# Optimization experiments

Measured on AMD Instinct MI355X. Metric: run time of the kernel, lower is better.

## Reference

```python
import jax, jax.numpy as jnp
import numpy as np

N, E = 40000, 640000
EMB, HID, H, TXT = 128, 128, 4, 384
C = HID // H  # per-head channels = 32


def _prelu(x, a):
    return jnp.where(x >= 0, x, a * x)


def _layernorm(x, g, b, eps=1e-5):
    m = jnp.mean(x, axis=-1, keepdims=True)
    v = jnp.mean((x - m) ** 2, axis=-1, keepdims=True)
    return (x - m) / jnp.sqrt(v + eps) * g + b


def _gat_conv(h, src, dst, W, att_src, att_dst, bias):
    # PyG GATConv (concat=True, eval mode): lin has no bias, self-loops already in src/dst.
    xh = (h @ W.T).reshape(N, H, C)                      # [N,H,C]
    a_src = jnp.sum(xh * att_src, axis=-1)               # [N,H]
    a_dst = jnp.sum(xh * att_dst, axis=-1)               # [N,H]
    alpha = jax.nn.leaky_relu(a_src[src] + a_dst[dst], negative_slope=0.2)  # [Et,H]
    amax = jax.ops.segment_max(alpha, dst, num_segments=N)
    ex = jnp.exp(alpha - amax[dst])
    denom = jax.ops.segment_sum(ex, dst, num_segments=N)
    coef = ex / denom[dst]                               # scatter-softmax over dst
    out = jax.ops.segment_sum(xh[src] * coef[:, :, None], dst, num_segments=N)
    return out.reshape(N, H * C) + bias


def setup_inputs() -> dict:
    key = jax.random.key(0)
    ks = jax.random.split(key, 20)
    nrm = lambda k, s, sc=0.05: jax.random.normal(k, s, jnp.float32) * sc
    inp = {
        "x": nrm(ks[0], (N, EMB), 1.0),
        "num_x": nrm(ks[1], (N, 1), 1.0),
        "num_mask": jnp.ones((N,), jnp.float32),
        "txt_x": nrm(ks[2], (N, TXT), 1.0),
        "txt_mask": jnp.ones((N,), jnp.float32),
        "edge_index": jax.random.randint(ks[3], (2, E), 0, N, jnp.int32),
        "num_proj_w": nrm(ks[4], (EMB, 1)), "num_proj_b": jnp.zeros((EMB,), jnp.float32),
        "txt_proj_w": nrm(ks[5], (EMB, TXT)), "txt_proj_b": jnp.zeros((EMB,), jnp.float32),
        "node_proj_w": nrm(ks[6], (HID, EMB)), "node_proj_b": jnp.zeros((HID,), jnp.float32),
        "prelu0_a": jnp.full((HID,), 0.25, jnp.float32),
        "conv1_w": nrm(ks[7], (HID, HID)), "att_src1": nrm(ks[8], (H, C)), "att_dst1": nrm(ks[9], (H, C)), "bias1": jnp.zeros((HID,), jnp.float32),
        "norm1_g": jnp.ones((HID,), jnp.float32), "norm1_b": jnp.zeros((HID,), jnp.float32),
        "prelu1_a": jnp.full((HID,), 0.25, jnp.float32),
        "conv2_w": nrm(ks[10], (HID, HID)), "att_src2": nrm(ks[11], (H, C)), "att_dst2": nrm(ks[12], (H, C)), "bias2": jnp.zeros((HID,), jnp.float32),
        "norm2_g": jnp.ones((HID,), jnp.float32), "norm2_b": jnp.zeros((HID,), jnp.float32),
        "prelu2_a": jnp.full((HID,), 0.25, jnp.float32),
        "out_w": nrm(ks[13], (1, HID)), "out_b": jnp.zeros((1,), jnp.float32),
    }
    return inp


def reference(x, num_x, num_mask, txt_x, txt_mask, edge_index,
              num_proj_w, num_proj_b, txt_proj_w, txt_proj_b,
              node_proj_w, node_proj_b, prelu0_a,
              conv1_w, att_src1, att_dst1, bias1, norm1_g, norm1_b, prelu1_a,
              conv2_w, att_src2, att_dst2, bias2, norm2_g, norm2_b, prelu2_a,
              out_w, out_b):
    # add self loops (PyG GATConv default)
    loop = jnp.arange(N, dtype=edge_index.dtype)
    src = jnp.concatenate([edge_index[0], loop])
    dst = jnp.concatenate([edge_index[1], loop])

    h = (num_x * num_mask[:, None]) @ num_proj_w.T + num_proj_b
    h = h + (txt_x * txt_mask[:, None]) @ txt_proj_w.T + txt_proj_b
    h = h + x @ node_proj_w.T + node_proj_b
    h = _prelu(h, prelu0_a)

    h = _gat_conv(h, src, dst, conv1_w, att_src1, att_dst1, bias1)
    h = _prelu(_layernorm(h, norm1_g, norm1_b), prelu1_a)  # dropout: eval mode -> identity

    h = _gat_conv(h, src, dst, conv2_w, att_src2, att_dst2, bias2)
    h = _prelu(_layernorm(h, norm2_g, norm2_b), prelu2_a)

    return (h @ out_w.T + out_b).squeeze(-1)  # [N]
```

## Files before the change

### kernel.cpp

```cpp
#include <hip/hip_runtime.h>
#include <stdint.h>

typedef unsigned short u16;
typedef unsigned int u32;
typedef __attribute__((ext_vector_type(8))) short bf16x8;
typedef __attribute__((ext_vector_type(4))) float f32x4;

__device__ __forceinline__ float bf2f(u32 u) {
    union { u32 i; float f; } v; v.i = u << 16; return v.f;
}
__device__ __forceinline__ u16 f2bf(float f) {
    u32 x = __float_as_uint(f);
    return (u16)((x + 0x7fffu + ((x >> 16) & 1u)) >> 16);
}
__device__ __forceinline__ float wred_sum(float v) {
#pragma unroll
    for (int o = 32; o > 0; o >>= 1) v += __shfl_xor(v, o, 64);
    return v;
}
__device__ __forceinline__ bf16x8 cvt8(float4 a, float4 b) {
    union { uint4 u; bf16x8 v; } t;
    t.u.x = (u32)f2bf(a.x) | ((u32)f2bf(a.y) << 16);
    t.u.y = (u32)f2bf(a.z) | ((u32)f2bf(a.w) << 16);
    t.u.z = (u32)f2bf(b.x) | ((u32)f2bf(b.y) << 16);
    t.u.w = (u32)f2bf(b.z) | ((u32)f2bf(b.w) << 16);
    return t.v;
}
__device__ __forceinline__ bf16x8 ld16B(const u16* p, size_t off) {
    union { uint4 u; bf16x8 b; } t; t.u = *(const uint4*)(p + off); return t.b;
}
__device__ __forceinline__ bf16x8 ldB(const u16* sw, int ct, int ks, int l16, int quad) {
    union { uint4 u; bf16x8 b; } t;
    t.u = *(const uint4*)&sw[(ct * 16 + l16) * 136 + ks * 32 + quad * 8];
    return t.b;
}
__device__ __forceinline__ void ldW8(const u16* __restrict__ W, int ldk, int koff,
                                     int tid, uint4* r) {
#pragma unroll
    for (int it = 0; it < 8; ++it) {
        int idx = (it * 256 + tid) * 8;
        int row = idx >> 7, kk = idx & 127;
        r[it] = *(const uint4*)(W + (size_t)row * ldk + koff + kk);
    }
}
__device__ __forceinline__ void stW8(u16* sw, int tid, const uint4* r) {
#pragma unroll
    for (int it = 0; it < 8; ++it) {
        int idx = (it * 256 + tid) * 8;
        int row = idx >> 7, kk = idx & 127;
        *(uint4*)&sw[row * 136 + kk] = r[it];
    }
}
__device__ __forceinline__ void ldA8(const float* __restrict__ p, float4* r) {
#pragma unroll
    for (int ks = 0; ks < 4; ++ks) {
        r[ks * 2]     = *(const float4*)(p + ks * 32);
        r[ks * 2 + 1] = *(const float4*)(p + ks * 32 + 4);
    }
}

__global__ void k_cvtw(const float* __restrict__ s0, const float* __restrict__ s1,
                       const float* __restrict__ s2, const float* __restrict__ s3,
                       u16* __restrict__ d, int n0, int n1, int n2, int n3) {
    int i = (blockIdx.x * 256 + threadIdx.x) * 8;
    int t = i;
    const float* s;
    if (t < n0) s = s0 + t;
    else if ((t -= n0) < n1) s = s1 + t;
    else if ((t -= n1) < n2) s = s2 + t;
    else if ((t -= n2) < n3) s = s3 + t;
    else return;
    float4 a = *(const float4*)s, b = *(const float4*)(s + 4);
    uint4 v;
    v.x = (u32)f2bf(a.x) | ((u32)f2bf(a.y) << 16);
    v.y = (u32)f2bf(a.z) | ((u32)f2bf(a.w) << 16);
    v.z = (u32)f2bf(b.x) | ((u32)f2bf(b.y) << 16);
    v.w = (u32)f2bf(b.z) | ((u32)f2bf(b.w) << 16);
    *(uint4*)(d + i) = v;
}

__global__ void k_zero(int* __restrict__ p, int n) {
    int i = blockIdx.x * 256 + threadIdx.x;
    if (i < n) p[i] = 0;
}
__global__ void k_hist(const int* __restrict__ dst, int E, int* __restrict__ deg) {
    int e = blockIdx.x * 256 + threadIdx.x;
    if (e < E) atomicAdd(&deg[dst[e]], 1);
}
__global__ __launch_bounds__(1024) void k_scanA(const int* __restrict__ deg, int n,
                                                int* __restrict__ out, int* __restrict__ bsum) {
    __shared__ int wsum[16];
    int t = threadIdx.x, w = t >> 6, lane = t & 63;
    int i0 = blockIdx.x * 4096 + t * 4;
    int4 v = make_int4(0, 0, 0, 0);
    if (i0 + 3 < n) v = *(const int4*)&deg[i0];
    else {
        if (i0 < n)     v.x = deg[i0];
        if (i0 + 1 < n) v.y = deg[i0 + 1];
        if (i0 + 2 < n) v.z = deg[i0 + 2];
    }
    int tsum = v.x + v.y + v.z + v.w;
    int s = tsum;
#pragma unroll
    for (int o = 1; o < 64; o <<= 1) { int u = __shfl_up(s, o, 64); if (lane >= o) s += u; }
    if (lane == 63) wsum[w] = s;
    __syncthreads();
    if (w == 0 && lane < 16) {
        int ws = wsum[lane];
#pragma unroll
        for (int o = 1; o < 16; o <<= 1) { int u = __shfl_up(ws, o, 64); if (lane >= o) ws += u; }
        wsum[lane] = ws;
    }
    __syncthreads();
    int woff = (w == 0) ? 0 : wsum[w - 1];
    int p = woff + s - tsum;
    if (i0 + 3 < n) {
        int4 o4; o4.x = p; o4.y = p + v.x; o4.z = p + v.x + v.y; o4.w = p + v.x + v.y + v.z;
        *(int4*)&out[i0] = o4;
    } else {
        int pp = p;
        if (i0 < n)     { out[i0] = pp;     pp += v.x; }
        if (i0 + 1 < n) { out[i0 + 1] = pp; pp += v.y; }
        if (i0 + 2 < n) { out[i0 + 2] = pp; }
    }
    if (t == 0) bsum[blockIdx.x] = wsum[15];
}
__global__ void k_scanB(int* __restrict__ bsum, int nb, int* __restrict__ total) {
    int lane = threadIdx.x;
    int v = (lane < nb) ? bsum[lane] : 0;
    int s = v;
#pragma unroll
    for (int o = 1; o < 64; o <<= 1) { int u = __shfl_up(s, o, 64); if (lane >= o) s += u; }
    if (lane < nb) bsum[lane] = s - v;
    if (lane == 63) total[0] = s;
}
__global__ void k_scanC(int* __restrict__ rowptr, int* __restrict__ cursor,
                        const int* __restrict__ boff, int n) {
    int i = blockIdx.x * 256 + threadIdx.x;
    if (i < n) {
        int r = rowptr[i] + boff[i >> 12];
        rowptr[i] = r; cursor[i] = r;
    }
}
__global__ void k_scatter(const int* __restrict__ srcp, const int* __restrict__ dstp, int E,
                          int* __restrict__ cursor, int* __restrict__ col) {
    int e = blockIdx.x * 256 + threadIdx.x;
    if (e < E) {
        int p = atomicAdd(&cursor[dstp[e]], 1);
        col[p] = srcp[e];
    }
}

__global__ __launch_bounds__(256, 1) void k_fused1(
    const float* __restrict__ x, const float* __restrict__ numx, const float* __restrict__ numm,
    const float* __restrict__ txt, const float* __restrict__ txtm,
    const float* __restrict__ numw, const float* __restrict__ numb,
    const float* __restrict__ txtb, const float* __restrict__ nodeb,
    const float* __restrict__ pa,
    const u16* __restrict__ txtwb, const u16* __restrict__ nodewb, const u16* __restrict__ w1b,
    const float* __restrict__ atts, const float* __restrict__ attd,
    u16* __restrict__ xh, float* __restrict__ asrc, float* __restrict__ adst) {
    __shared__ u16 sw[128 * 136];
    __shared__ u16 sh[4][16 * 136];
    int tid = threadIdx.x, w = tid >> 6, lane = tid & 63, quad = lane >> 4, l16 = lane & 15;
    int nb = blockIdx.x * 64 + w * 16;

    const float* trow = txt + (size_t)(nb + l16) * 384 + quad * 8;
    const float* xrow = x + (size_t)(nb + l16) * 128 + quad * 8;

    f32x4 acc[8];
#pragma unroll
    for (int ct = 0; ct < 8; ++ct) { f32x4 z = {0.f, 0.f, 0.f, 0.f}; acc[ct] = z; }

    auto compute = [&](const float4* A) {
#pragma unroll
        for (int ks = 0; ks < 4; ++ks) {
            bf16x8 a0 = cvt8(A[ks * 2], A[ks * 2 + 1]);
#pragma unroll
            for (int ct = 0; ct < 8; ++ct)
                acc[ct] = __builtin_amdgcn_mfma_f32_16x16x32_bf16(
                    a0, ldB(sw, ct, ks, l16, quad), acc[ct], 0, 0, 0);
        }
    };

    uint4 w0[8], w1[8], w2[8];
    float4 aC[8], aN[8];

    ldW8(txtwb, 384, 0, tid, w0);
    ldW8(txtwb, 384, 128, tid, w1);
    ldA8(trow, aC);

    stW8(sw, tid, w0);
    __syncthreads();
    ldW8(txtwb, 384, 256, tid, w2);
    ldA8(trow + 128, aN);
    compute(aC);
    __syncthreads();

    stW8(sw, tid, w1);
    __syncthreads();
    ldW8(nodewb, 128, 0, tid, w0);
    ldA8(trow + 256, aC);
    compute(aN);
    __syncthreads();

    stW8(sw, tid, w2);
    __syncthreads();
    ldW8(w1b, 128, 0, tid, w1);
    ldA8(xrow, aN);
    compute(aC);
#pragma unroll
    for (int r = 0; r < 4; ++r) {
        float tm = txtm[nb + quad * 4 + r];
#pragma unroll
        for (int ct = 0; ct < 8; ++ct) acc[ct][r] *= tm;
    }
    __syncthreads();

    stW8(sw, tid, w0);
    __syncthreads();
    compute(aN);

    float nm[4];
#pragma unroll
    for (int r = 0; r < 4; ++r) {
        int n = nb + quad * 4 + r;
        nm[r] = numx[n] * numm[n];
    }
#pragma unroll
    for (int ct = 0; ct < 8; ++ct) {
        int c = ct * 16 + l16;
        float cw = numw[c];
        float cb = numb[c] + txtb[c] + nodeb[c];
        float pav = pa[c];
#pragma unroll
        for (int r = 0; r < 4; ++r) {
            float v = acc[ct][r] + nm[r] * cw + cb;
            v = v >= 0.f ? v : pav * v;
            sh[w][(quad * 4 + r) * 136 + c] = f2bf(v);
        }
    }
    __syncthreads();
    stW8(sw, tid, w1);
    __syncthreads();
    f32x4 a2[8];
#pragma unroll
    for (int ct = 0; ct < 8; ++ct) { f32x4 z = {0.f, 0.f, 0.f, 0.f}; a2[ct] = z; }
#pragma unroll
    for (int ks = 0; ks < 4; ++ks) {
        bf16x8 a0 = ld16B(sh[w], l16 * 136 + ks * 32 + quad * 8);
#pragma unroll
        for (int ct = 0; ct < 8; ++ct)
            a2[ct] = __builtin_amdgcn_mfma_f32_16x16x32_bf16(
                a0, ldB(sw, ct, ks, l16, quad), a2[ct], 0, 0, 0);
    }
#pragma unroll
    for (int ct = 0; ct < 8; ++ct) {
        int c = ct * 16 + l16;
#pragma unroll
        for (int r = 0; r < 4; ++r)
            xh[(size_t)(nb + quad * 4 + r) * 128 + c] = f2bf(a2[ct][r]);
    }
    float as_[8], ad_[8];
#pragma unroll
    for (int ct = 0; ct < 8; ++ct) {
        int c = ct * 16 + l16;
        as_[ct] = atts[c];
        ad_[ct] = attd[c];
    }
#pragma unroll
    for (int hh = 0; hh < 4; ++hh) {
        float vs[4], vd[4];
#pragma unroll
        for (int r = 0; r < 4; ++r) {
            vs[r] = a2[2 * hh][r] * as_[2 * hh] + a2[2 * hh + 1][r] * as_[2 * hh + 1];
            vd[r] = a2[2 * hh][r] * ad_[2 * hh] + a2[2 * hh + 1][r] * ad_[2 * hh + 1];
        }
#pragma unroll
        for (int o = 1; o <= 8; o <<= 1) {
#pragma unroll
            for (int r = 0; r < 4; ++r) {
                vs[r] += __shfl_xor(vs[r], o, 64);
                vd[r] += __shfl_xor(vd[r], o, 64);
            }
        }
        if ((l16 >> 2) == hh) {
            int r = l16 & 3;
            float ss = (r == 0) ? vs[0] : (r == 1) ? vs[1] : (r == 2) ? vs[2] : vs[3];
            float dd = (r == 0) ? vd[0] : (r == 1) ? vd[1] : (r == 2) ? vd[2] : vd[3];
            int n = nb + quad * 4 + r;
            asrc[n * 4 + hh] = ss;
            adst[n * 4 + hh] = dd;
        }
    }
}

__global__ __launch_bounds__(256) void k_xh(
    const u16* __restrict__ h, const u16* __restrict__ Wb,
    const float* __restrict__ att_s, const float* __restrict__ att_d,
    u16* __restrict__ xh, float* __restrict__ asrc, float* __restrict__ adst) {
    __shared__ u16 sw[128 * 136];
    int tid = threadIdx.x;
    int w = tid >> 6, lane = tid & 63, quad = lane >> 4, l16 = lane & 15;
    int nb = blockIdx.x * 64 + w * 16;
    uint4 wr[8];
    ldW8(Wb, 128, 0, tid, wr);
    uint4 Ar[4];
    const u16* hrow = h + (size_t)(nb + l16) * 128;
#pragma unroll
    for (int ks = 0; ks < 4; ++ks) Ar[ks] = *(const uint4*)(hrow + ks * 32 + quad * 8);
    f32x4 acc[8];
#pragma unroll
    for (int ct = 0; ct < 8; ++ct) { f32x4 z = {0.f, 0.f, 0.f, 0.f}; acc[ct] = z; }
    stW8(sw, tid, wr);
    __syncthreads();
#pragma unroll
    for (int ks = 0; ks < 4; ++ks) {
        union { uint4 u; bf16x8 b; } t; t.u = Ar[ks];
#pragma unroll
        for (int ct = 0; ct < 8; ++ct)
            acc[ct] = __builtin_amdgcn_mfma_f32_16x16x32_bf16(
                t.b, ldB(sw, ct, ks, l16, quad), acc[ct], 0, 0, 0);
    }
#pragma unroll
    for (int ct = 0; ct < 8; ++ct) {
        int c = ct * 16 + l16;
#pragma unroll
        for (int r = 0; r < 4; ++r) {
            int n = nb + quad * 4 + r;
            xh[(size_t)n * 128 + c] = f2bf(acc[ct][r]);
        }
    }
    float as_[8], ad_[8];
#pragma unroll
    for (int ct = 0; ct < 8; ++ct) {
        int c = ct * 16 + l16;
        as_[ct] = att_s[c];
        ad_[ct] = att_d[c];
    }
#pragma unroll
    for (int hh = 0; hh < 4; ++hh) {
        float vs[4], vd[4];
#pragma unroll
        for (int r = 0; r < 4; ++r) {
            vs[r] = acc[2 * hh][r] * as_[2 * hh] + acc[2 * hh + 1][r] * as_[2 * hh + 1];
            vd[r] = acc[2 * hh][r] * ad_[2 * hh] + acc[2 * hh + 1][r] * ad_[2 * hh + 1];
        }
#pragma unroll
        for (int o = 1; o <= 8; o <<= 1) {
#pragma unroll
            for (int r = 0; r < 4; ++r) {
                vs[r] += __shfl_xor(vs[r], o, 64);
                vd[r] += __shfl_xor(vd[r], o, 64);
            }
        }
        if ((l16 >> 2) == hh) {
            int r = l16 & 3;
            float ss = (r == 0) ? vs[0] : (r == 1) ? vs[1] : (r == 2) ? vs[2] : vs[3];
            float dd = (r == 0) ? vd[0] : (r == 1) ? vd[1] : (r == 2) ? vd[2] : vd[3];
            int n = nb + quad * 4 + r;
            asrc[n * 4 + hh] = ss;
            adst[n * 4 + hh] = dd;
        }
    }
}

__global__ __launch_bounds__(64) void k_agg(
    const u16* __restrict__ xh, const float* __restrict__ asrc, const float* __restrict__ adst,
    const int* __restrict__ rowptr, const int* __restrict__ col,
    const float* __restrict__ bias, const float* __restrict__ g, const float* __restrict__ b,
    const float* __restrict__ pa, u16* __restrict__ hnext,
    const float* __restrict__ outw, const float* __restrict__ outb, float* __restrict__ outy,
    int is_final) {
    __shared__ int   scol[64];
    __shared__ float scoef[64][4];
    int n = blockIdx.x, lane = threadIdx.x;
    int beg = rowptr[n], end = rowptr[n + 1];
    const float4* asrc4 = (const float4*)asrc;

    float4 adv = ((const float4*)adst)[n];
    float ad[4] = { adv.x, adv.y, adv.z, adv.w };
    float4 asv = asrc4[n];
    float els[4];
#pragma unroll
    for (int h = 0; h < 4; h++) {
        float a = ((const float*)&asv)[h] + ad[h];
        a = a >= 0.f ? a : 0.2f * a;
        els[h] = __expf(a);
    }
    int hh = lane >> 4;
    u32 vself = ((const u32*)(xh + (size_t)n * 128))[lane];
    float ac0[8], ac1[8];
#pragma unroll
    for (int q = 0; q < 8; ++q) { ac0[q] = 0.f; ac1[q] = 0.f; }
    ac0[0] = els[hh] * bf2f(vself & 0xffffu);
    ac1[0] = els[hh] * bf2f(vself >> 16);
    float l[4] = { 0.f, 0.f, 0.f, 0.f };

    for (int base = beg; base < end; base += 64) {
        int e = base + lane;
        int cnt = min(64, end - base);
        if (e < end) {
            int s = col[e];
            float4 av = asrc4[s];
            scol[lane] = s;
            float cf[4];
#pragma unroll
            for (int h = 0; h < 4; h++) {
                float a = ((const float*)&av)[h] + ad[h];
                a = a >= 0.f ? a : 0.2f * a;
                cf[h] = __expf(a);
                l[h] += cf[h];
            }
            *(float4*)scoef[lane] = make_float4(cf[0], cf[1], cf[2], cf[3]);
        }
        __syncthreads();
        int j = 0;
        for (; j + 7 < cnt; j += 8) {
            int ss[8]; float cc[8]; u32 vv[8];
#pragma unroll
            for (int q = 0; q < 8; ++q) { ss[q] = scol[j + q]; cc[q] = scoef[j + q][hh]; }
#pragma unroll
            for (int q = 0; q < 8; ++q) vv[q] = ((const u32*)(xh + (size_t)ss[q] * 128))[lane];
#pragma unroll
            for (int q = 0; q < 8; ++q) {
                ac0[q] += cc[q] * bf2f(vv[q] & 0xffffu);
                ac1[q] += cc[q] * bf2f(vv[q] >> 16);
            }
        }
        for (; j + 3 < cnt; j += 4) {
            int ss[4]; float cc[4]; u32 vv[4];
#pragma unroll
            for (int q = 0; q < 4; ++q) { ss[q] = scol[j + q]; cc[q] = scoef[j + q][hh]; }
#pragma unroll
            for (int q = 0; q < 4; ++q) vv[q] = ((const u32*)(xh + (size_t)ss[q] * 128))[lane];
#pragma unroll
            for (int q = 0; q < 4; ++q) {
                ac0[q] += cc[q] * bf2f(vv[q] & 0xffffu);
                ac1[q] += cc[q] * bf2f(vv[q] >> 16);
            }
        }
        for (; j < cnt; ++j) {
            int s0 = scol[j];
            float c0 = scoef[j][hh];
            u32 v0 = ((const u32*)(xh + (size_t)s0 * 128))[lane];
            ac0[0] += c0 * bf2f(v0 & 0xffffu);
            ac1[0] += c0 * bf2f(v0 >> 16);
        }
        __syncthreads();
    }
    float acc0 = 0.f, acc1 = 0.f;
#pragma unroll
    for (int q = 0; q < 8; ++q) { acc0 += ac0[q]; acc1 += ac1[q]; }

    float L[4];
#pragma unroll
    for (int h = 0; h < 4; h++) L[h] = wred_sum(l[h]) + els[h];
    float inv = 1.f / L[hh];
    acc0 *= inv;
    acc1 *= inv;

    int c0i = 2 * lane;
    float2 bi = *(const float2*)(bias + c0i);
    acc0 += bi.x; acc1 += bi.y;

    float mean = wred_sum(acc0 + acc1) * (1.f / 128.f);
    float d0 = acc0 - mean, d1 = acc1 - mean;
    float var = wred_sum(d0 * d0 + d1 * d1) * (1.f / 128.f);
    float rstd = rsqrtf(var + 1e-5f);
    float2 gg = *(const float2*)(g + c0i);
    float2 bb = *(const float2*)(b + c0i);
    float2 pp = *(const float2*)(pa + c0i);
    float y0 = d0 * rstd * gg.x + bb.x;
    float y1 = d1 * rstd * gg.y + bb.y;
    y0 = y0 >= 0.f ? y0 : pp.x * y0;
    y1 = y1 >= 0.f ? y1 : pp.y * y1;

    if (is_final) {
        float2 ow = *(const float2*)(outw + c0i);
        float dot = wred_sum(y0 * ow.x + y1 * ow.y);
        if (lane == 0) outy[n] = dot + outb[0];
    } else {
        ((u32*)(hnext + (size_t)n * 128))[lane] = (u32)f2bf(y0) | ((u32)f2bf(y1) << 16);
    }
}

extern "C" void kernel_launch(void* const* d_in, const int* in_sizes, int n_in,
                              void* d_out, int out_size, void* d_ws, size_t ws_size,
                              hipStream_t stream) {
    const int N = in_sizes[2];
    const int E = in_sizes[5] / 2;

    const float* x      = (const float*)d_in[0];
    const float* numx   = (const float*)d_in[1];
    const float* numm   = (const float*)d_in[2];
    const float* txt    = (const float*)d_in[3];
    const float* txtm   = (const float*)d_in[4];
    const int*   ei     = (const int*)d_in[5];
    const float* numw   = (const float*)d_in[6];
    const float* numb   = (const float*)d_in[7];
    const float* txtw   = (const float*)d_in[8];
    const float* txtb   = (const float*)d_in[9];
    const float* nodew  = (const float*)d_in[10];
    const float* nodeb  = (const float*)d_in[11];
    const float* pa0    = (const float*)d_in[12];
    const float* conv1w = (const float*)d_in[13];
    const float* atts1  = (const float*)d_in[14];
    const float* attd1  = (const float*)d_in[15];
    const float* bias1  = (const float*)d_in[16];
    const float* g1     = (const float*)d_in[17];
    const float* b1     = (const float*)d_in[18];
    const float* pa1    = (const float*)d_in[19];
    const float* conv2w = (const float*)d_in[20];
    const float* atts2  = (const float*)d_in[21];
    const float* attd2  = (const float*)d_in[22];
    const float* bias2  = (const float*)d_in[23];
    const float* g2     = (const float*)d_in[24];
    const float* b2     = (const float*)d_in[25];
    const float* pa2    = (const float*)d_in[26];
    const float* outw   = (const float*)d_in[27];
    const float* outb   = (const float*)d_in[28];

    const int* srcp = ei;
    const int* dstp = ei + E;

    const int szTxtw = in_sizes[8];
    const int szNode = in_sizes[10];
    const int szW1   = in_sizes[13];
    const int szW2   = in_sizes[20];
    const int szWAll = szTxtw + szNode + szW1 + szW2;

    char* p = (char*)d_ws;
    auto alloc = [&](size_t bytes) -> void* {
        void* q = (void*)p;
        p += (bytes + 255) & ~(size_t)255;
        return q;
    };
    u16*   hA     = (u16*)alloc((size_t)N * 128 * 2);
    u16*   hB     = (u16*)alloc((size_t)N * 128 * 2);
    float* asrc   = (float*)alloc((size_t)N * 4 * 4);
    float* adst   = (float*)alloc((size_t)N * 4 * 4);
    int*   deg    = (int*)alloc((size_t)N * 4);
    int*   rowptr = (int*)alloc((size_t)(N + 1) * 4);
    int*   cursor = (int*)alloc((size_t)N * 4);
    int*   col    = (int*)alloc((size_t)E * 4);
    int*   bsum   = (int*)alloc(64 * 4);
    u16*   wbf    = (u16*)alloc((size_t)szWAll * 2);

    u16* txtwb  = wbf;
    u16* nodewb = wbf + szTxtw;
    u16* w1b    = nodewb + szNode;
    u16* w2b    = w1b + szW1;

    k_cvtw<<<(szWAll / 8 + 255) / 256, 256, 0, stream>>>(
        txtw, nodew, conv1w, conv2w, wbf, szTxtw, szNode, szW1, szW2);

    const int nbScan = (N + 4095) / 4096;
    k_zero<<<(N + 255) / 256, 256, 0, stream>>>(deg, N);
    k_hist<<<(E + 255) / 256, 256, 0, stream>>>(dstp, E, deg);
    k_scanA<<<nbScan, 1024, 0, stream>>>(deg, N, rowptr, bsum);
    k_scanB<<<1, 64, 0, stream>>>(bsum, nbScan, rowptr + N);
    k_scanC<<<(N + 255) / 256, 256, 0, stream>>>(rowptr, cursor, bsum, N);
    k_scatter<<<(E + 255) / 256, 256, 0, stream>>>(srcp, dstp, E, cursor, col);

    const int gProj = N / 64;

    k_fused1<<<gProj, 256, 0, stream>>>(x, numx, numm, txt, txtm, numw, numb,
                                        txtb, nodeb, pa0,
                                        txtwb, nodewb, w1b, atts1, attd1, hB, asrc, adst);
    k_agg<<<N, 64, 0, stream>>>(hB, asrc, adst, rowptr, col, bias1, g1, b1, pa1,
                                hA, nullptr, nullptr, nullptr, 0);

    k_xh<<<gProj, 256, 0, stream>>>(hA, w2b, atts2, attd2, hB, asrc, adst);
    k_agg<<<N, 64, 0, stream>>>(hB, asrc, adst, rowptr, col, bias2, g2, b2, pa2,
                                nullptr, outw, outb, (float*)d_out, 1);
}
```

Baseline: 357.4 us.

## Stage GEMM weights via direct global-to-LDS loads with XOR-swizzled layout

Replaces register-staged weight loads (global→VGPR→LDS) with global_load_lds direct copies into an unpadded LDS tile using an XOR swizzle to avoid bank conflicts. This applies to the fused projection kernel and the per-layer xh kernel. It drops the register double-buffering of weights and A rows and removes launch_bounds(256,1), so more blocks can be resident per CU. In exchange, prefetch overlap across chunks is lost: each chunk now loads, syncs, computes, then syncs again.

```diff
diff --git a/kernel.cpp b/kernel.cpp
--- a/kernel.cpp
+++ b/kernel.cpp
@@ -29,34 +29,30 @@
 __device__ __forceinline__ bf16x8 ld16B(const u16* p, size_t off) {
     union { uint4 u; bf16x8 b; } t; t.u = *(const uint4*)(p + off); return t.b;
 }
-__device__ __forceinline__ bf16x8 ldB(const u16* sw, int ct, int ks, int l16, int quad) {
+__device__ __forceinline__ void glds16(const void* g, void* l) {
+    __builtin_amdgcn_global_load_lds(
+        (const __attribute__((address_space(1))) void*)g,
+        (__attribute__((address_space(3))) void*)l, 16, 0, 0);
+}
+__device__ __forceinline__ void stageW_glds(const u16* __restrict__ W, int ldk, int koff,
+                                            u16* swl, int tid) {
+    int w64 = tid >> 6;
+#pragma unroll
+    for (int it = 0; it < 8; ++it) {
+        int row = it * 16 + (tid >> 4);
+        int sphys = tid & 15;
+        int ssrc = sphys ^ (row & 7);
+        const u16* g = W + (size_t)row * ldk + koff + ssrc * 8;
+        u16* dst = swl + (size_t)(it * 256 + w64 * 64) * 8;
+        glds16(g, dst);
+    }
+}
+__device__ __forceinline__ bf16x8 ldBx(const u16* swl, int ct, int ks, int l16, int quad) {
+    int row = ct * 16 + l16;
+    int slot = (ks * 4 + quad) ^ (row & 7);
     union { uint4 u; bf16x8 b; } t;
-    t.u = *(const uint4*)&sw[(ct * 16 + l16) * 136 + ks * 32 + quad * 8];
+    t.u = *(const uint4*)&swl[row * 128 + slot * 8];
     return t.b;
-}
-__device__ __forceinline__ void ldW8(const u16* __restrict__ W, int ldk, int koff,
-                                     int tid, uint4* r) {
-#pragma unroll
-    for (int it = 0; it < 8; ++it) {
-        int idx = (it * 256 + tid) * 8;
-        int row = idx >> 7, kk = idx & 127;
-        r[it] = *(const uint4*)(W + (size_t)row * ldk + koff + kk);
-    }
-}
-__device__ __forceinline__ void stW8(u16* sw, int tid, const uint4* r) {
-#pragma unroll
-    for (int it = 0; it < 8; ++it) {
-        int idx = (it * 256 + tid) * 8;
-        int row = idx >> 7, kk = idx & 127;
-        *(uint4*)&sw[row * 136 + kk] = r[it];
-    }
-}
-__device__ __forceinline__ void ldA8(const float* __restrict__ p, float4* r) {
-#pragma unroll
-    for (int ks = 0; ks < 4; ++ks) {
-        r[ks * 2]     = *(const float4*)(p + ks * 32);
-        r[ks * 2 + 1] = *(const float4*)(p + ks * 32 + 4);
-    }
 }
 
 __global__ void k_cvtw(const float* __restrict__ s0, const float* __restrict__ s1,
@@ -151,7 +147,7 @@
     }
 }
 
-__global__ __launch_bounds__(256, 1) void k_fused1(
+__global__ __launch_bounds__(256) void k_fused1(
     const float* __restrict__ x, const float* __restrict__ numx, const float* __restrict__ numm,
     const float* __restrict__ txt, const float* __restrict__ txtm,
     const float* __restrict__ numw, const float* __restrict__ numb,
@@ -160,7 +156,7 @@
     const u16* __restrict__ txtwb, const u16* __restrict__ nodewb, const u16* __restrict__ w1b,
     const float* __restrict__ atts, const float* __restrict__ attd,
     u16* __restrict__ xh, float* __restrict__ asrc, float* __restrict__ adst) {
-    __shared__ u16 sw[128 * 136];
+    __shared__ u16 swl[128 * 128];
     __shared__ u16 sh[4][16 * 136];
     int tid = threadIdx.x, w = tid >> 6, lane = tid & 63, quad = lane >> 4, l16 = lane & 15;
     int nb = blockIdx.x * 64 + w * 16;
@@ -172,54 +168,47 @@
 #pragma unroll
     for (int ct = 0; ct < 8; ++ct) { f32x4 z = {0.f, 0.f, 0.f, 0.f}; acc[ct] = z; }
 
-    auto compute = [&](const float4* A) {
-#pragma unroll
-        for (int ks = 0; ks < 4; ++ks) {
-            bf16x8 a0 = cvt8(A[ks * 2], A[ks * 2 + 1]);
-#pragma unroll
-            for (int ct = 0; ct < 8; ++ct)
-                acc[ct] = __builtin_amdgcn_mfma_f32_16x16x32_bf16(
-                    a0, ldB(sw, ct, ks, l16, quad), acc[ct], 0, 0, 0);
-        }
-    };
-
-    uint4 w0[8], w1[8], w2[8];
-    float4 aC[8], aN[8];
-
-    ldW8(txtwb, 384, 0, tid, w0);
-    ldW8(txtwb, 384, 128, tid, w1);
-    ldA8(trow, aC);
-
-    stW8(sw, tid, w0);
-    __syncthreads();
-    ldW8(txtwb, 384, 256, tid, w2);
-    ldA8(trow + 128, aN);
-    compute(aC);
-    __syncthreads();
-
-    stW8(sw, tid, w1);
-    __syncthreads();
-    ldW8(nodewb, 128, 0, tid, w0);
-    ldA8(trow + 256, aC);
-    compute(aN);
-    __syncthreads();
-
-    stW8(sw, tid, w2);
-    __syncthreads();
-    ldW8(w1b, 128, 0, tid, w1);
-    ldA8(xrow, aN);
-    compute(aC);
+#define CHUNK(Wp, ldk, koff, Ap)                                               \
+    {                                                                          \
+        stageW_glds(Wp, ldk, koff, swl, tid);                                  \
+        const float* pA_ = (Ap);                                               \
+        float4 A0 = *(const float4*)(pA_ + 0),  A1 = *(const float4*)(pA_ + 4);  \
+        float4 A2 = *(const float4*)(pA_ + 32), A3 = *(const float4*)(pA_ + 36); \
+        float4 A4 = *(const float4*)(pA_ + 64), A5 = *(const float4*)(pA_ + 68); \
+        float4 A6 = *(const float4*)(pA_ + 96), A7 = *(const float4*)(pA_ + 100);\
+        __syncthreads();                 \
+        bf16x8 f0 = cvt8(A0, A1), f1 = cvt8(A2, A3);                           \
+        bf16x8 f2 = cvt8(A4, A5), f3 = cvt8(A6, A7);                           \
+        _Pragma("unroll")                                                      \
+        for (int ct = 0; ct < 8; ++ct)                                         \
+            acc[ct] = __builtin_amdgcn_mfma_f32_16x16x32_bf16(                 \
+                f0, ldBx(swl, ct, 0, l16, quad), acc[ct], 0, 0, 0);            \
+        _Pragma("unroll")                                                      \
+        for (int ct = 0; ct < 8; ++ct)                                         \
+            acc[ct] = __builtin_amdgcn_mfma_f32_16x16x32_bf16(                 \
+                f1, ldBx(swl, ct, 1, l16, quad), acc[ct], 0, 0, 0);            \
+        _Pragma("unroll")                                                      \
+        for (int ct = 0; ct < 8; ++ct)                                         \
+            acc[ct] = __builtin_amdgcn_mfma_f32_16x16x32_bf16(                 \
+                f2, ldBx(swl, ct, 2, l16, quad), acc[ct], 0, 0, 0);            \
+        _Pragma("unroll")                                                      \
+        for (int ct = 0; ct < 8; ++ct)                                         \
+            acc[ct] = __builtin_amdgcn_mfma_f32_16x16x32_bf16(                 \
+                f3, ldBx(swl, ct, 3, l16, quad), acc[ct], 0, 0, 0);            \
+        __syncthreads();                       \
+    }
+
+    CHUNK(txtwb, 384, 0,   trow)
+    CHUNK(txtwb, 384, 128, trow + 128)
+    CHUNK(txtwb, 384, 256, trow + 256)
 #pragma unroll
     for (int r = 0; r < 4; ++r) {
         float tm = txtm[nb + quad * 4 + r];
 #pragma unroll
         for (int ct = 0; ct < 8; ++ct) acc[ct][r] *= tm;
     }
-    __syncthreads();
-
-    stW8(sw, tid, w0);
-    __syncthreads();
-    compute(aN);
+    CHUNK(nodewb, 128, 0, xrow)
+#undef CHUNK
 
     float nm[4];
 #pragma unroll
@@ -241,7 +230,7 @@
         }
     }
     __syncthreads();
-    stW8(sw, tid, w1);
+    stageW_glds(w1b, 128, 0, swl, tid);
     __syncthreads();
     f32x4 a2[8];
 #pragma unroll
@@ -252,7 +241,7 @@
 #pragma unroll
         for (int ct = 0; ct < 8; ++ct)
             a2[ct] = __builtin_amdgcn_mfma_f32_16x16x32_bf16(
-                a0, ldB(sw, ct, ks, l16, quad), a2[ct], 0, 0, 0);
+                a0, ldBx(swl, ct, ks, l16, quad), a2[ct], 0, 0, 0);
     }
 #pragma unroll
     for (int ct = 0; ct < 8; ++ct) {
@@ -299,29 +288,39 @@
     const u16* __restrict__ h, const u16* __restrict__ Wb,
     const float* __restrict__ att_s, const float* __restrict__ att_d,
     u16* __restrict__ xh, float* __restrict__ asrc, float* __restrict__ adst) {
-    __shared__ u16 sw[128 * 136];
+    __shared__ u16 swl[128 * 128];
     int tid = threadIdx.x;
     int w = tid >> 6, lane = tid & 63, quad = lane >> 4, l16 = lane & 15;
     int nb = blockIdx.x * 64 + w * 16;
-    uint4 wr[8];
-    ldW8(Wb, 128, 0, tid, wr);
-    uint4 Ar[4];
-    const u16* hrow = h + (size_t)(nb + l16) * 128;
-#pragma unroll
-    for (int ks = 0; ks < 4; ++ks) Ar[ks] = *(const uint4*)(hrow + ks * 32 + quad * 8);
+
+    stageW_glds(Wb, 128, 0, swl, tid);
+    const u16* hrow = h + (size_t)(nb + l16) * 128 + quad * 8;
+    uint4 A0 = *(const uint4*)(hrow);
+    uint4 A1 = *(const uint4*)(hrow + 32);
+    uint4 A2 = *(const uint4*)(hrow + 64);
+    uint4 A3 = *(const uint4*)(hrow + 96);
     f32x4 acc[8];
 #pragma unroll
     for (int ct = 0; ct < 8; ++ct) { f32x4 z = {0.f, 0.f, 0.f, 0.f}; acc[ct] = z; }
-    stW8(sw, tid, wr);
     __syncthreads();
-#pragma unroll
-    for (int ks = 0; ks < 4; ++ks) {
-        union { uint4 u; bf16x8 b; } t; t.u = Ar[ks];
-#pragma unroll
-        for (int ct = 0; ct < 8; ++ct)
-            acc[ct] = __builtin_amdgcn_mfma_f32_16x16x32_bf16(
-                t.b, ldB(sw, ct, ks, l16, quad), acc[ct], 0, 0, 0);
-    }
+    union { uint4 u; bf16x8 b; } t0, t1, t2, t3;
+    t0.u = A0; t1.u = A1; t2.u = A2; t3.u = A3;
+#pragma unroll
+    for (int ct = 0; ct < 8; ++ct)
+        acc[ct] = __builtin_amdgcn_mfma_f32_16x16x32_bf16(
+            t0.b, ldBx(swl, ct, 0, l16, quad), acc[ct], 0, 0, 0);
+#pragma unroll
+    for (int ct = 0; ct < 8; ++ct)
+        acc[ct] = __builtin_amdgcn_mfma_f32_16x16x32_bf16(
+            t1.b, ldBx(swl, ct, 1, l16, quad), acc[ct], 0, 0, 0);
+#pragma unroll
+    for (int ct = 0; ct < 8; ++ct)
+        acc[ct] = __builtin_amdgcn_mfma_f32_16x16x32_bf16(
+            t2.b, ldBx(swl, ct, 2, l16, quad), acc[ct], 0, 0, 0);
+#pragma unroll
+    for (int ct = 0; ct < 8; ++ct)
+        acc[ct] = __builtin_amdgcn_mfma_f32_16x16x32_bf16(
+            t3.b, ldBx(swl, ct, 3, l16, quad), acc[ct], 0, 0, 0);
 #pragma unroll
     for (int ct = 0; ct < 8; ++ct) {
         int c = ct * 16 + l16;
```

After: 323.4 us. 1.11x faster.
